# Kernel tuning notes

Measured on AMD Instinct MI355X. Metric: run time of the kernel, lower is better.

Reference implementation:

```python
import jax, jax.numpy as jnp
import numpy as np

B, N, IN_DIM, HID = 16, 2048, 128, 128
EPS = 1e-5


def _layer(x, W, b, g, beta):
    # x: (B, N, d_in) -> (B, N, HID)
    h = jnp.einsum('bnd,dh->bnh', x, W) + b
    mu = jnp.mean(h, axis=-1, keepdims=True)
    var = jnp.mean((h - mu) ** 2, axis=-1, keepdims=True)
    h = (h - mu) * jax.lax.rsqrt(var + EPS) * g + beta
    return jax.nn.relu(h)


def setup_inputs() -> dict:
    key = jax.random.key(0)
    ks = jax.random.split(key, 8)
    x = jax.random.normal(ks[0], (B, N, IN_DIM), dtype=jnp.float32)
    adj = jax.random.uniform(ks[1], (B, N, N), dtype=jnp.float32)
    inp = {'x': x, 'adj': adj}
    dims = [IN_DIM, HID, HID]
    for i in range(3):
        d_in = dims[i]
        scale = 1.0 / np.sqrt(d_in)
        inp[f'W{i}'] = jax.random.uniform(ks[2 + i], (d_in, HID), dtype=jnp.float32, minval=-scale, maxval=scale)
        inp[f'b{i}'] = jax.random.uniform(ks[5 + i], (HID,), dtype=jnp.float32, minval=-scale, maxval=scale)
        inp[f'g{i}'] = jnp.ones((HID,), dtype=jnp.float32)
        inp[f'be{i}'] = jnp.zeros((HID,), dtype=jnp.float32)
    return inp


def reference(x, adj, W0, b0, g0, be0, W1, b1, g1, be1, W2, b2, g2, be2):
    params = [(W0, b0, g0, be0), (W1, b1, g1, be1), (W2, b2, g2, be2)]
    h = x
    for (W, b, g, beta) in params:
        h_agg = jnp.einsum('bnm,bmd->bnd', adj, h)  # dense adjacency aggregation
        h = _layer(h_agg, W, b, g, beta)
    return h
```

## Files before the change

kernel.cpp:

```cpp
#include <hip/hip_runtime.h>
#include <hip/hip_bf16.h>

typedef __bf16 bf16;
typedef __bf16 bf16x4 __attribute__((ext_vector_type(4)));
typedef __bf16 bf16x8 __attribute__((ext_vector_type(8)));
typedef float  f32x2  __attribute__((ext_vector_type(2)));
typedef float  f32x4  __attribute__((ext_vector_type(4)));

static constexpr int NB  = 16;
static constexpr int NN  = 2048;
static constexpr int HID = 128;

__device__ __forceinline__ void gload_lds16(const bf16* g, bf16* l) {
    __builtin_amdgcn_global_load_lds(
        (const __attribute__((address_space(1))) unsigned int*)g,
        (__attribute__((address_space(3))) unsigned int*)l, 16, 0, 0);
}

__global__ __launch_bounds__(256) void prep_wt(const float* __restrict__ W0,
                                               const float* __restrict__ W1,
                                               const float* __restrict__ W2,
                                               bf16* __restrict__ WT) {
    int l = blockIdx.x;
    const float* W = (l == 0) ? W0 : (l == 1) ? W1 : W2;
    bf16* out = WT + l * 128 * 128;
    int tid = threadIdx.x;
#pragma unroll
    for (int i = 0; i < 64; ++i) {
        int idx = i * 256 + tid;
        int k = idx >> 7, n = idx & 127;
        out[n * 128 + k] = (bf16)W[idx];
    }
}

__global__ __launch_bounds__(256) void prep_xt(const float* __restrict__ x,
                                               bf16* __restrict__ xT) {
    __shared__ bf16 T[128 * 136];
    const int blk = blockIdx.x;
    const int b = blk >> 4, node0 = (blk & 15) * 128;
    const int tid = threadIdx.x;
    const float* xb = x + ((size_t)b * NN + node0) * HID;
#pragma unroll
    for (int i = 0; i < 64; ++i) {
        int idx = i * 256 + tid;
        int node = idx >> 7, hid = idx & 127;
        T[hid * 136 + node] = (bf16)xb[(size_t)node * HID + hid];
    }
    __syncthreads();
    bf16* ob = xT + (size_t)b * HID * NN + node0;
#pragma unroll
    for (int i = 0; i < 8; ++i) {
        int flat = i * 2048 + tid * 8;
        int hid = flat >> 7, node = flat & 127;
        *(bf16x8*)(ob + (size_t)hid * NN + node) = *(const bf16x8*)(T + hid * 136 + node);
    }
}

template<int AMODE>
__global__ __launch_bounds__(256, 2) void big_gemm(const float* __restrict__ Af,
                                                   bf16* __restrict__ adjB,
                                                   const bf16* __restrict__ Bt,
                                                   bf16* __restrict__ g) {
    __shared__ bf16 As[64 * 64];
    __shared__ bf16 Bs[128 * 64];

    const int tid  = threadIdx.x;
    const int wave = tid >> 6, lane = tid & 63;
    const int c0 = lane & 15, q = lane >> 4;
    const int m0 = blockIdx.x * 64;
    const int b  = blockIdx.z;
    const size_t abase = (size_t)b * NN * NN;
    const bf16* Btb = Bt + (size_t)b * HID * NN;
    const int wm = wave >> 1, wn = wave & 1;

    f32x4 acc[2][4] = {};

    int prow[4], pcb[4];
#pragma unroll
    for (int j = 0; j < 4; ++j) {
        int p = j * 256 + wave * 64 + lane;
        prow[j] = p >> 3;
        pcb[j]  = (p & 7) ^ (prow[j] & 7);
    }
    const int ldsbase = wave * 512;

    for (int kk = 0; kk < 32; ++kk) {
        const int k0 = kk * 64;
        if constexpr (AMODE == 1) {
#pragma unroll
            for (int j = 0; j < 2; ++j) {
                int gi = j * 256 + tid;
                int grow = gi >> 3, gcb = gi & 7;
                const float* src = Af + abase + (size_t)(m0 + grow) * NN + k0 + gcb * 8;
                f32x4 a  = *(const f32x4*)src;
                f32x4 b2 = *(const f32x4*)(src + 4);
                bf16x8 o = {(bf16)a.x, (bf16)a.y, (bf16)a.z, (bf16)a.w,
                            (bf16)b2.x, (bf16)b2.y, (bf16)b2.z, (bf16)b2.w};
                *(bf16x8*)(As + (grow * 8 + (gcb ^ (grow & 7))) * 8) = o;
                *(bf16x8*)(adjB + abase + (size_t)(m0 + grow) * NN + k0 + gcb * 8) = o;
            }
        } else {
#pragma unroll
            for (int j = 0; j < 2; ++j)
                gload_lds16(adjB + abase + (size_t)(m0 + prow[j]) * NN + k0 + pcb[j] * 8,
                            As + j * 2048 + ldsbase);
        }
#pragma unroll
        for (int j = 0; j < 4; ++j)
            gload_lds16(Btb + (size_t)prow[j] * NN + k0 + pcb[j] * 8,
                        Bs + j * 2048 + ldsbase);
        __syncthreads();
#pragma unroll
        for (int ks = 0; ks < 2; ++ks) {
            bf16x8 af[2], bfr[4];
#pragma unroll
            for (int mt = 0; mt < 2; ++mt) {
                int row = wm * 32 + mt * 16 + c0;
                int cb  = (ks * 4 + q) ^ (row & 7);
                af[mt] = *(const bf16x8*)(As + row * 64 + cb * 8);
            }
#pragma unroll
            for (int nt = 0; nt < 4; ++nt) {
                int row = wn * 64 + nt * 16 + c0;
                int cb  = (ks * 4 + q) ^ (row & 7);
                bfr[nt] = *(const bf16x8*)(Bs + row * 64 + cb * 8);
            }
#pragma unroll
            for (int mt = 0; mt < 2; ++mt)
#pragma unroll
                for (int nt = 0; nt < 4; ++nt)
                    acc[mt][nt] = __builtin_amdgcn_mfma_f32_16x16x32_bf16(af[mt], bfr[nt], acc[mt][nt], 0, 0, 0);
        }
        __syncthreads();
    }

    bf16* gb = g + ((size_t)b * NN + m0) * HID;
#pragma unroll
    for (int mt = 0; mt < 2; ++mt)
#pragma unroll
        for (int r = 0; r < 4; ++r) {
            int m = wm * 32 + mt * 16 + q * 4 + r;
#pragma unroll
            for (int nt = 0; nt < 4; ++nt) {
                int n = wn * 64 + nt * 16 + c0;
                gb[(size_t)m * HID + n] = (bf16)acc[mt][nt][r];
            }
        }
}

template<bool FINAL>
__global__ __launch_bounds__(256) void small_ln(const bf16* __restrict__ gin,
                                                const bf16* __restrict__ WT,
                                                const float* __restrict__ bias,
                                                const float* __restrict__ gamma,
                                                const float* __restrict__ betap,
                                                bf16* __restrict__ hT,
                                                float* __restrict__ outF) {
    __shared__ bf16 smem[2 * 128 * 72];
    bf16* As = smem;
    bf16* Bs = smem + 128 * 72;

    const int tid  = threadIdx.x;
    const int wave = tid >> 6, lane = tid & 63;
    const int c0 = lane & 15, q = lane >> 4;
    const int blk = blockIdx.x;
    const int row_g0 = blk * 128;

    f32x4 acc[2][8] = {};

    for (int kk = 0; kk < 2; ++kk) {
        const int k0 = kk * 64;
#pragma unroll
        for (int i = 0; i < 4; ++i) {
            int flat = i * 2048 + tid * 8;
            int row = flat >> 6, col = flat & 63;
            bf16x8 v = *(const bf16x8*)(gin + (size_t)(row_g0 + row) * HID + k0 + col);
            *(bf16x8*)(As + row * 72 + col) = v;
        }
#pragma unroll
        for (int i = 0; i < 4; ++i) {
            int flat = i * 2048 + tid * 8;
            int row = flat >> 6, col = flat & 63;
            bf16x8 v = *(const bf16x8*)(WT + (size_t)row * 128 + k0 + col);
            *(bf16x8*)(Bs + row * 72 + col) = v;
        }
        __syncthreads();
#pragma unroll
        for (int ks = 0; ks < 2; ++ks) {
            bf16x8 af[2];
#pragma unroll
            for (int mt = 0; mt < 2; ++mt)
                af[mt] = *(const bf16x8*)(As + (wave * 32 + mt * 16 + c0) * 72 + ks * 32 + q * 8);
#pragma unroll
            for (int nt = 0; nt < 8; ++nt) {
                bf16x8 bfr = *(const bf16x8*)(Bs + (nt * 16 + c0) * 72 + ks * 32 + q * 8);
#pragma unroll
                for (int mt = 0; mt < 2; ++mt)
                    acc[mt][nt] = __builtin_amdgcn_mfma_f32_16x16x32_bf16(af[mt], bfr, acc[mt][nt], 0, 0, 0);
            }
        }
        __syncthreads();
    }

    float bv[8], gv[8], bev[8];
#pragma unroll
    for (int nt = 0; nt < 8; ++nt) {
        int n = nt * 16 + c0;
        bv[nt] = bias[n]; gv[nt] = gamma[n]; bev[nt] = betap[n];
    }
    bf16* Cs = smem;
#pragma unroll
    for (int mt = 0; mt < 2; ++mt) {
#pragma unroll
        for (int r = 0; r < 4; ++r) {
            float v[8], s1 = 0.f, s2 = 0.f;
#pragma unroll
            for (int nt = 0; nt < 8; ++nt) {
                float xv = acc[mt][nt][r] + bv[nt];
                v[nt] = xv; s1 += xv; s2 += xv * xv;
            }
#pragma unroll
            for (int off = 1; off < 16; off <<= 1) {
                s1 += __shfl_xor(s1, off);
                s2 += __shfl_xor(s2, off);
            }
            float mu  = s1 * (1.f / 128.f);
            float var = s2 * (1.f / 128.f) - mu * mu;
            float rs  = rsqrtf(var + 1e-5f);
            int m = wave * 32 + mt * 16 + q * 4 + r;
            if constexpr (FINAL) {
                size_t rowoff = ((size_t)row_g0 + m) * HID;
#pragma unroll
                for (int nt = 0; nt < 8; ++nt) {
                    float o = fmaxf((v[nt] - mu) * rs * gv[nt] + bev[nt], 0.f);
                    outF[rowoff + nt * 16 + c0] = o;
                }
            } else {
#pragma unroll
                for (int nt = 0; nt < 8; ++nt) {
                    float o = fmaxf((v[nt] - mu) * rs * gv[nt] + bev[nt], 0.f);
                    Cs[(nt * 16 + c0) * 136 + m] = (bf16)o;
                }
            }
        }
    }
    if constexpr (!FINAL) {
        __syncthreads();
        const int b = blk >> 4, row0 = (blk & 15) * 128;
        bf16* outp = hT + (size_t)b * HID * NN;
#pragma unroll
        for (int i = 0; i < 8; ++i) {
            int flat = i * 2048 + tid * 8;
            int n = flat >> 7, mm = flat & 127;
            *(bf16x8*)(outp + (size_t)n * NN + row0 + mm) = *(const bf16x8*)(Cs + n * 136 + mm);
        }
    }
}

extern "C" void kernel_launch(void* const* d_in, const int* in_sizes, int n_in,
                              void* d_out, int out_size, void* d_ws, size_t ws_size,
                              hipStream_t stream) {
    const float* x   = (const float*)d_in[0];
    const float* adj = (const float*)d_in[1];
    const float* W[3]  = {(const float*)d_in[2],  (const float*)d_in[6],  (const float*)d_in[10]};
    const float* bb[3] = {(const float*)d_in[3],  (const float*)d_in[7],  (const float*)d_in[11]};
    const float* gg[3] = {(const float*)d_in[4],  (const float*)d_in[8],  (const float*)d_in[12]};
    const float* be[3] = {(const float*)d_in[5],  (const float*)d_in[9],  (const float*)d_in[13]};

    char* ws = (char*)d_ws;
    size_t off = 0;
    auto alloc = [&](size_t bytes) { char* p = ws + off; off = (off + bytes + 255) & ~(size_t)255; return p; };
    bf16* WT   = (bf16*)alloc((size_t)3 * 128 * 128 * 2);
    bf16* xT   = (bf16*)alloc((size_t)NB * HID * NN * 2);
    bf16* hT   = (bf16*)alloc((size_t)NB * HID * NN * 2);
    bf16* gbuf = (bf16*)alloc((size_t)NB * NN * HID * 2);
    bf16* adjB = (bf16*)alloc((size_t)NB * NN * NN * 2);

    float* outF = (float*)d_out;

    prep_wt<<<3, 256, 0, stream>>>(W[0], W[1], W[2], WT);
    prep_xt<<<256, 256, 0, stream>>>(x, xT);

    dim3 bg(32, 1, 16);
    big_gemm<1><<<bg, 256, 0, stream>>>(adj, adjB, xT, gbuf);
    small_ln<false><<<256, 256, 0, stream>>>(gbuf, WT, bb[0], gg[0], be[0], hT, nullptr);
    big_gemm<2><<<bg, 256, 0, stream>>>(adj, adjB, hT, gbuf);
    small_ln<false><<<256, 256, 0, stream>>>(gbuf, WT + 128 * 128, bb[1], gg[1], be[1], hT, nullptr);
    big_gemm<2><<<bg, 256, 0, stream>>>(adj, adjB, hT, gbuf);
    small_ln<true><<<256, 256, 0, stream>>>(gbuf, WT + 2 * 128 * 128, bb[2], gg[2], be[2], nullptr, outF);
}
```

Baseline: 552.4 us.

## Double-buffer big_gemm LDS tiles and remap blocks so each XCD owns two batches

The adjacency GEMM now keeps two LDS stages, so the next K tile's global loads (async for bf16 adj and B, register-staged for the fp32 first pass) are issued before computing on the current tile. This is meant to hide load latency that was previously serialized behind a barrier. The grid also becomes 1D with a mapping that puts blocks of the same two batches on one XCD, aiming for better L2 reuse of the B operand. Doubling LDS use to 48KB per block may cut how many blocks fit per CU, and the fp32 path holds more registers across the compute step.

Result: no change. 555.5 us (+0.6%).

```diff
diff --git a/kernel.cpp b/kernel.cpp
--- a/kernel.cpp
+++ b/kernel.cpp
@@ -61,14 +61,18 @@
                                                    bf16* __restrict__ adjB,
                                                    const bf16* __restrict__ Bt,
                                                    bf16* __restrict__ g) {
-    __shared__ bf16 As[64 * 64];
-    __shared__ bf16 Bs[128 * 64];
+    __shared__ bf16 As[2][64 * 64];
+    __shared__ bf16 Bs[2][128 * 64];
 
     const int tid  = threadIdx.x;
     const int wave = tid >> 6, lane = tid & 63;
     const int c0 = lane & 15, q = lane >> 4;
-    const int m0 = blockIdx.x * 64;
-    const int b  = blockIdx.z;
+
+    const int blk = blockIdx.x;
+    const int xcd = blk & 7, jj = blk >> 3;
+    const int b   = xcd * 2 + (jj & 1);
+    const int m0  = (jj >> 1) * 64;
+
     const size_t abase = (size_t)b * NN * NN;
     const bf16* Btb = Bt + (size_t)b * HID * NN;
     const int wm = wave >> 1, wn = wave & 1;
@@ -84,32 +88,44 @@
     }
     const int ldsbase = wave * 512;
 
-    for (int kk = 0; kk < 32; ++kk) {
-        const int k0 = kk * 64;
-        if constexpr (AMODE == 1) {
-#pragma unroll
-            for (int j = 0; j < 2; ++j) {
-                int gi = j * 256 + tid;
-                int grow = gi >> 3, gcb = gi & 7;
-                const float* src = Af + abase + (size_t)(m0 + grow) * NN + k0 + gcb * 8;
-                f32x4 a  = *(const f32x4*)src;
-                f32x4 b2 = *(const f32x4*)(src + 4);
-                bf16x8 o = {(bf16)a.x, (bf16)a.y, (bf16)a.z, (bf16)a.w,
-                            (bf16)b2.x, (bf16)b2.y, (bf16)b2.z, (bf16)b2.w};
-                *(bf16x8*)(As + (grow * 8 + (gcb ^ (grow & 7))) * 8) = o;
-                *(bf16x8*)(adjB + abase + (size_t)(m0 + grow) * NN + k0 + gcb * 8) = o;
-            }
-        } else {
-#pragma unroll
-            for (int j = 0; j < 2; ++j)
-                gload_lds16(adjB + abase + (size_t)(m0 + prow[j]) * NN + k0 + pcb[j] * 8,
-                            As + j * 2048 + ldsbase);
-        }
+    int grow_[2], gcb_[2];
+#pragma unroll
+    for (int j = 0; j < 2; ++j) {
+        int gi = j * 256 + tid;
+        grow_[j] = gi >> 3;
+        gcb_[j]  = gi & 7;
+    }
+
+    auto stageB = [&](int buf, int k0) {
 #pragma unroll
         for (int j = 0; j < 4; ++j)
             gload_lds16(Btb + (size_t)prow[j] * NN + k0 + pcb[j] * 8,
-                        Bs + j * 2048 + ldsbase);
-        __syncthreads();
+                        &Bs[buf][j * 2048 + ldsbase]);
+    };
+    auto stageA_async = [&](int buf, int k0) {
+#pragma unroll
+        for (int j = 0; j < 2; ++j)
+            gload_lds16(adjB + abase + (size_t)(m0 + prow[j]) * NN + k0 + pcb[j] * 8,
+                        &As[buf][j * 2048 + ldsbase]);
+    };
+    auto loadA_f32 = [&](int k0, f32x4* va, f32x4* vb) {
+#pragma unroll
+        for (int j = 0; j < 2; ++j) {
+            const float* src = Af + abase + (size_t)(m0 + grow_[j]) * NN + k0 + gcb_[j] * 8;
+            va[j] = *(const f32x4*)src;
+            vb[j] = *(const f32x4*)(src + 4);
+        }
+    };
+    auto writeA = [&](int buf, int k0, const f32x4* va, const f32x4* vb) {
+#pragma unroll
+        for (int j = 0; j < 2; ++j) {
+            bf16x8 o = {(bf16)va[j].x, (bf16)va[j].y, (bf16)va[j].z, (bf16)va[j].w,
+                        (bf16)vb[j].x, (bf16)vb[j].y, (bf16)vb[j].z, (bf16)vb[j].w};
+            *(bf16x8*)(&As[buf][(grow_[j] * 8 + (gcb_[j] ^ (grow_[j] & 7))) * 8]) = o;
+            *(bf16x8*)(adjB + abase + (size_t)(m0 + grow_[j]) * NN + k0 + gcb_[j] * 8) = o;
+        }
+    };
+    auto compute = [&](int buf) {
 #pragma unroll
         for (int ks = 0; ks < 2; ++ks) {
             bf16x8 af[2], bfr[4];
@@ -117,13 +133,13 @@
             for (int mt = 0; mt < 2; ++mt) {
                 int row = wm * 32 + mt * 16 + c0;
                 int cb  = (ks * 4 + q) ^ (row & 7);
-                af[mt] = *(const bf16x8*)(As + row * 64 + cb * 8);
+                af[mt] = *(const bf16x8*)(&As[buf][row * 64 + cb * 8]);
             }
 #pragma unroll
             for (int nt = 0; nt < 4; ++nt) {
                 int row = wn * 64 + nt * 16 + c0;
                 int cb  = (ks * 4 + q) ^ (row & 7);
-                bfr[nt] = *(const bf16x8*)(Bs + row * 64 + cb * 8);
+                bfr[nt] = *(const bf16x8*)(&Bs[buf][row * 64 + cb * 8]);
             }
 #pragma unroll
             for (int mt = 0; mt < 2; ++mt)
@@ -131,7 +147,39 @@
                 for (int nt = 0; nt < 4; ++nt)
                     acc[mt][nt] = __builtin_amdgcn_mfma_f32_16x16x32_bf16(af[mt], bfr[nt], acc[mt][nt], 0, 0, 0);
         }
+    };
+
+    f32x4 va[2], vb[2];
+    if constexpr (AMODE == 1) {
+        loadA_f32(0, va, vb);
+        stageB(0, 0);
+        writeA(0, 0, va, vb);
+    } else {
+        stageA_async(0, 0);
+        stageB(0, 0);
+    }
+    __syncthreads();
+
+    int cur = 0;
+    for (int kk = 0; kk < 32; ++kk) {
+        const int k1 = (kk + 1) * 64;
+        if constexpr (AMODE == 1) {
+            if (kk < 31) {
+                loadA_f32(k1, va, vb);
+                stageB(cur ^ 1, k1);
+            }
+            compute(cur);
+            if (kk < 31)
+                writeA(cur ^ 1, k1, va, vb);
+        } else {
+            if (kk < 31) {
+                stageA_async(cur ^ 1, k1);
+                stageB(cur ^ 1, k1);
+            }
+            compute(cur);
+        }
         __syncthreads();
+        cur ^= 1;
     }
 
     bf16* gb = g + ((size_t)b * NN + m0) * HID;
@@ -281,11 +329,10 @@
     prep_wt<<<3, 256, 0, stream>>>(W[0], W[1], W[2], WT);
     prep_xt<<<256, 256, 0, stream>>>(x, xT);
 
-    dim3 bg(32, 1, 16);
-    big_gemm<1><<<bg, 256, 0, stream>>>(adj, adjB, xT, gbuf);
+    big_gemm<1><<<512, 256, 0, stream>>>(adj, adjB, xT, gbuf);
     small_ln<false><<<256, 256, 0, stream>>>(gbuf, WT, bb[0], gg[0], be[0], hT, nullptr);
-    big_gemm<2><<<bg, 256, 0, stream>>>(adj, adjB, hT, gbuf);
+    big_gemm<2><<<512, 256, 0, stream>>>(adj, adjB, hT, gbuf);
     small_ln<false><<<256, 256, 0, stream>>>(gbuf, WT + 128 * 128, bb[1], gg[1], be[1], hT, nullptr);
-    big_gemm<2><<<bg, 256, 0, stream>>>(adj, adjB, hT, gbuf);
+    big_gemm<2><<<512, 256, 0, stream>>>(adj, adjB, hT, gbuf);
     small_ln<true><<<256, 256, 0, stream>>>(gbuf, WT + 2 * 128 * 128, bb[2], gg[2], be[2], nullptr, outF);
 }
```

## Fuse aggregation GEMM with weight GEMM and LayerNorm per layer, pre-swizzled tiles

Applied to the files above, without the earlier changes.

Merges the adjacency aggregation GEMM and the small weight-GEMM plus LayerNorm/ReLU into one kernel per layer, so the intermediate g tensor stays in LDS instead of going through global memory. Operands are stored in a pre-tiled, pre-swizzled layout so each 64-wide K chunk is one contiguous block that global_load_lds can copy directly. Loads are double-buffered with explicit vmcnt waits, and blocks are mapped by XCD for cache locality. Tiles grow to 128 rows with 512 threads, which raises LDS use and may lower occupancy.

Result: faster. 494.7 us (-10.4%).

```diff
diff --git a/kernel.cpp b/kernel.cpp
--- a/kernel.cpp
+++ b/kernel.cpp
@@ -2,9 +2,7 @@
 #include <hip/hip_bf16.h>
 
 typedef __bf16 bf16;
-typedef __bf16 bf16x4 __attribute__((ext_vector_type(4)));
 typedef __bf16 bf16x8 __attribute__((ext_vector_type(8)));
-typedef float  f32x2  __attribute__((ext_vector_type(2)));
 typedef float  f32x4  __attribute__((ext_vector_type(4)));
 
 static constexpr int NB  = 16;
@@ -16,25 +14,32 @@
         (const __attribute__((address_space(1))) unsigned int*)g,
         (__attribute__((address_space(3))) unsigned int*)l, 16, 0, 0);
 }
+__device__ __forceinline__ void memfence() { asm volatile("" ::: "memory"); }
+
 
 __global__ __launch_bounds__(256) void prep_wt(const float* __restrict__ W0,
                                                const float* __restrict__ W1,
                                                const float* __restrict__ W2,
-                                               bf16* __restrict__ WT) {
+                                               bf16* __restrict__ WTg) {
     int l = blockIdx.x;
     const float* W = (l == 0) ? W0 : (l == 1) ? W1 : W2;
-    bf16* out = WT + l * 128 * 128;
+    bf16* out = WTg + l * 16384;
     int tid = threadIdx.x;
 #pragma unroll
-    for (int i = 0; i < 64; ++i) {
-        int idx = i * 256 + tid;
-        int k = idx >> 7, n = idx & 127;
-        out[n * 128 + k] = (bf16)W[idx];
+    for (int i = 0; i < 8; ++i) {
+        int p = i * 256 + tid;
+        int n = p >> 4, half = (p >> 3) & 1, cs = p & 7;
+        int kc = cs ^ (n & 7);
+        int kbase = half * 64 + kc * 8;
+        bf16x8 o;
+#pragma unroll
+        for (int r = 0; r < 8; ++r) o[r] = (bf16)W[(kbase + r) * 128 + n];
+        *(bf16x8*)(out + p * 8) = o;
     }
 }
 
 __global__ __launch_bounds__(256) void prep_xt(const float* __restrict__ x,
-                                               bf16* __restrict__ xT) {
+                                               bf16* __restrict__ xTt) {
     __shared__ bf16 T[128 * 136];
     const int blk = blockIdx.x;
     const int b = blk >> 4, node0 = (blk & 15) * 128;
@@ -47,212 +52,220 @@
         T[hid * 136 + node] = (bf16)xb[(size_t)node * HID + hid];
     }
     __syncthreads();
-    bf16* ob = xT + (size_t)b * HID * NN + node0;
 #pragma unroll
     for (int i = 0; i < 8; ++i) {
-        int flat = i * 2048 + tid * 8;
-        int hid = flat >> 7, node = flat & 127;
-        *(bf16x8*)(ob + (size_t)hid * NN + node) = *(const bf16x8*)(T + hid * 136 + node);
-    }
-}
-
-template<int AMODE>
-__global__ __launch_bounds__(256, 2) void big_gemm(const float* __restrict__ Af,
-                                                   bf16* __restrict__ adjB,
-                                                   const bf16* __restrict__ Bt,
-                                                   bf16* __restrict__ g) {
-    __shared__ bf16 As[64 * 64];
-    __shared__ bf16 Bs[128 * 64];
-
-    const int tid  = threadIdx.x;
-    const int wave = tid >> 6, lane = tid & 63;
+        int p = i * 256 + tid;
+        int half = p >> 10, p1 = p & 1023;
+        int n = p1 >> 3, cs = p1 & 7, c = cs ^ (n & 7), m = half * 64 + c * 8;
+        *(bf16x8*)(xTt + ((size_t)b * 32 + (node0 >> 6) + half) * 8192 + p1 * 8)
+            = *(const bf16x8*)(T + n * 136 + m);
+    }
+}
+
+template<int AMODE, bool FINAL>
+__global__ __launch_bounds__(512, 2) void fused_layer(
+        const float* __restrict__ Af, bf16* __restrict__ adjT,
+        const bf16* __restrict__ Bt, const bf16* __restrict__ WTg,
+        const float* __restrict__ bias, const float* __restrict__ gam,
+        const float* __restrict__ bet, bf16* __restrict__ hOut,
+        float* __restrict__ outF) {
+    __shared__ __align__(16) bf16 lds[49152];
+    bf16* WTl = lds + 32768;
+
+    const int tid = threadIdx.x, wave = tid >> 6, lane = tid & 63;
     const int c0 = lane & 15, q = lane >> 4;
-    const int m0 = blockIdx.x * 64;
-    const int b  = blockIdx.z;
-    const size_t abase = (size_t)b * NN * NN;
-    const bf16* Btb = Bt + (size_t)b * HID * NN;
+    const int blk = blockIdx.x, xcd = blk & 7, jj = blk >> 3;
+    const int b = xcd * 2 + (jj & 1);
+    const int mtile = jj >> 1, m0 = mtile * 128;
     const int wm = wave >> 1, wn = wave & 1;
 
+    const bf16* Btb = Bt + (size_t)b * 32 * 8192;
+    bf16* Atl = adjT + ((size_t)b * 16 + mtile) * 32 * 8192;
+
     f32x4 acc[2][4] = {};
 
-    int prow[4], pcb[4];
 #pragma unroll
     for (int j = 0; j < 4; ++j) {
-        int p = j * 256 + wave * 64 + lane;
-        prow[j] = p >> 3;
-        pcb[j]  = (p & 7) ^ (prow[j] & 7);
-    }
-    const int ldsbase = wave * 512;
-
-    for (int kk = 0; kk < 32; ++kk) {
-        const int k0 = kk * 64;
-        if constexpr (AMODE == 1) {
-#pragma unroll
-            for (int j = 0; j < 2; ++j) {
-                int gi = j * 256 + tid;
-                int grow = gi >> 3, gcb = gi & 7;
-                const float* src = Af + abase + (size_t)(m0 + grow) * NN + k0 + gcb * 8;
-                f32x4 a  = *(const f32x4*)src;
-                f32x4 b2 = *(const f32x4*)(src + 4);
-                bf16x8 o = {(bf16)a.x, (bf16)a.y, (bf16)a.z, (bf16)a.w,
-                            (bf16)b2.x, (bf16)b2.y, (bf16)b2.z, (bf16)b2.w};
-                *(bf16x8*)(As + (grow * 8 + (gcb ^ (grow & 7))) * 8) = o;
-                *(bf16x8*)(adjB + abase + (size_t)(m0 + grow) * NN + k0 + gcb * 8) = o;
-            }
-        } else {
-#pragma unroll
-            for (int j = 0; j < 2; ++j)
-                gload_lds16(adjB + abase + (size_t)(m0 + prow[j]) * NN + k0 + pcb[j] * 8,
-                            As + j * 2048 + ldsbase);
-        }
-#pragma unroll
-        for (int j = 0; j < 4; ++j)
-            gload_lds16(Btb + (size_t)prow[j] * NN + k0 + pcb[j] * 8,
-                        Bs + j * 2048 + ldsbase);
-        __syncthreads();
+        int cb = j * 512 + wave * 64;
+        gload_lds16(WTg + (size_t)(cb + lane) * 8, WTl + cb * 8);
+    }
+
+    auto stageA2 = [&](int buf, int kk) {
+#pragma unroll
+        for (int j = 0; j < 2; ++j) {
+            int cb = j * 512 + wave * 64;
+            gload_lds16(Atl + (size_t)kk * 8192 + (size_t)(cb + lane) * 8,
+                        lds + buf * 16384 + cb * 8);
+        }
+    };
+    auto stageB2 = [&](int buf, int kk) {
+#pragma unroll
+        for (int j = 0; j < 2; ++j) {
+            int cb = j * 512 + wave * 64;
+            gload_lds16(Btb + (size_t)kk * 8192 + (size_t)(cb + lane) * 8,
+                        lds + buf * 16384 + 8192 + cb * 8);
+        }
+    };
+    auto compute = [&](int buf) {
+        const bf16* As = lds + buf * 16384;
+        const bf16* Bs = As + 8192;
 #pragma unroll
         for (int ks = 0; ks < 2; ++ks) {
-            bf16x8 af[2], bfr[4];
+            bf16x8 af[2], bf_[4];
 #pragma unroll
             for (int mt = 0; mt < 2; ++mt) {
                 int row = wm * 32 + mt * 16 + c0;
-                int cb  = (ks * 4 + q) ^ (row & 7);
+                int cb = (ks * 4 + q) ^ (row & 7);
                 af[mt] = *(const bf16x8*)(As + row * 64 + cb * 8);
             }
 #pragma unroll
             for (int nt = 0; nt < 4; ++nt) {
                 int row = wn * 64 + nt * 16 + c0;
-                int cb  = (ks * 4 + q) ^ (row & 7);
-                bfr[nt] = *(const bf16x8*)(Bs + row * 64 + cb * 8);
+                int cb = (ks * 4 + q) ^ (row & 7);
+                bf_[nt] = *(const bf16x8*)(Bs + row * 64 + cb * 8);
             }
 #pragma unroll
             for (int mt = 0; mt < 2; ++mt)
 #pragma unroll
                 for (int nt = 0; nt < 4; ++nt)
-                    acc[mt][nt] = __builtin_amdgcn_mfma_f32_16x16x32_bf16(af[mt], bfr[nt], acc[mt][nt], 0, 0, 0);
-        }
+                    acc[mt][nt] = __builtin_amdgcn_mfma_f32_16x16x32_bf16(
+                        af[mt], bf_[nt], acc[mt][nt], 0, 0, 0);
+        }
+    };
+
+    if constexpr (AMODE == 1) {
+        int grow[2], gcb[2];
+#pragma unroll
+        for (int j = 0; j < 2; ++j) {
+            int gi = j * 512 + tid;
+            grow[j] = gi >> 3; gcb[j] = gi & 7;
+        }
+        f32x4 va[2], vb[2];
+        auto loadA = [&](int kk) {
+#pragma unroll
+            for (int j = 0; j < 2; ++j) {
+                const float* s = Af + (size_t)b * NN * NN
+                               + (size_t)(m0 + grow[j]) * NN + kk * 64 + gcb[j] * 8;
+                va[j] = *(const f32x4*)s;
+                vb[j] = *(const f32x4*)(s + 4);
+            }
+        };
+        auto writeA = [&](int buf, int kk) {
+#pragma unroll
+            for (int j = 0; j < 2; ++j) {
+                bf16x8 o = {(bf16)va[j].x, (bf16)va[j].y, (bf16)va[j].z, (bf16)va[j].w,
+                            (bf16)vb[j].x, (bf16)vb[j].y, (bf16)vb[j].z, (bf16)vb[j].w};
+                int ch = grow[j] * 8 + (gcb[j] ^ (grow[j] & 7));
+                *(bf16x8*)(lds + buf * 16384 + ch * 8) = o;
+                *(bf16x8*)(Atl + (size_t)kk * 8192 + ch * 8) = o;
+            }
+        };
+        loadA(0); stageB2(0, 0); writeA(0, 0);
         __syncthreads();
-    }
-
-    bf16* gb = g + ((size_t)b * NN + m0) * HID;
+        int cur = 0;
+        for (int kk = 0; kk < 32; ++kk) {
+            if (kk < 31) { loadA(kk + 1); stageB2(cur ^ 1, kk + 1); }
+            compute(cur);
+            if (kk < 31) writeA(cur ^ 1, kk + 1);
+            __syncthreads();
+            cur ^= 1;
+        }
+    } else {
+        stageA2(0, 0); stageB2(0, 0);
+        stageA2(1, 1); stageB2(1, 1);
+#pragma unroll 1
+        for (int kk = 0; kk < 32; ++kk) {
+            if (kk < 31) asm volatile("s_waitcnt vmcnt(4)" ::: "memory");
+            else         asm volatile("s_waitcnt vmcnt(0)" ::: "memory");
+            __builtin_amdgcn_s_barrier();
+            memfence();
+            compute(kk & 1);
+            memfence();
+            __builtin_amdgcn_s_barrier();
+            if (kk < 30) { stageA2(kk & 1, kk + 2); stageB2(kk & 1, kk + 2); }
+        }
+        __syncthreads();
+    }
+
+    bf16* G = lds;
 #pragma unroll
     for (int mt = 0; mt < 2; ++mt)
 #pragma unroll
         for (int r = 0; r < 4; ++r) {
-            int m = wm * 32 + mt * 16 + q * 4 + r;
+            int row = wm * 32 + mt * 16 + q * 4 + r;
 #pragma unroll
             for (int nt = 0; nt < 4; ++nt) {
-                int n = wn * 64 + nt * 16 + c0;
-                gb[(size_t)m * HID + n] = (bf16)acc[mt][nt][r];
-            }
-        }
-}
-
-template<bool FINAL>
-__global__ __launch_bounds__(256) void small_ln(const bf16* __restrict__ gin,
-                                                const bf16* __restrict__ WT,
-                                                const float* __restrict__ bias,
-                                                const float* __restrict__ gamma,
-                                                const float* __restrict__ betap,
-                                                bf16* __restrict__ hT,
-                                                float* __restrict__ outF) {
-    __shared__ bf16 smem[2 * 128 * 72];
-    bf16* As = smem;
-    bf16* Bs = smem + 128 * 72;
-
-    const int tid  = threadIdx.x;
-    const int wave = tid >> 6, lane = tid & 63;
-    const int c0 = lane & 15, q = lane >> 4;
-    const int blk = blockIdx.x;
-    const int row_g0 = blk * 128;
-
-    f32x4 acc[2][8] = {};
-
-    for (int kk = 0; kk < 2; ++kk) {
-        const int k0 = kk * 64;
-#pragma unroll
-        for (int i = 0; i < 4; ++i) {
-            int flat = i * 2048 + tid * 8;
-            int row = flat >> 6, col = flat & 63;
-            bf16x8 v = *(const bf16x8*)(gin + (size_t)(row_g0 + row) * HID + k0 + col);
-            *(bf16x8*)(As + row * 72 + col) = v;
-        }
-#pragma unroll
-        for (int i = 0; i < 4; ++i) {
-            int flat = i * 2048 + tid * 8;
-            int row = flat >> 6, col = flat & 63;
-            bf16x8 v = *(const bf16x8*)(WT + (size_t)row * 128 + k0 + col);
-            *(bf16x8*)(Bs + row * 72 + col) = v;
-        }
-        __syncthreads();
-#pragma unroll
-        for (int ks = 0; ks < 2; ++ks) {
-            bf16x8 af[2];
-#pragma unroll
-            for (int mt = 0; mt < 2; ++mt)
-                af[mt] = *(const bf16x8*)(As + (wave * 32 + mt * 16 + c0) * 72 + ks * 32 + q * 8);
+                int col = wn * 64 + nt * 16 + c0;
+                G[row * 136 + col] = (bf16)acc[mt][nt][r];
+            }
+        }
+    __syncthreads();
+
+    f32x4 a2[8] = {};
+    {
+        const int gr = wave * 16 + c0;
+#pragma unroll
+        for (int ks = 0; ks < 4; ++ks) {
+            bf16x8 af = *(const bf16x8*)(G + gr * 136 + ks * 32 + q * 8);
 #pragma unroll
             for (int nt = 0; nt < 8; ++nt) {
-                bf16x8 bfr = *(const bf16x8*)(Bs + (nt * 16 + c0) * 72 + ks * 32 + q * 8);
-#pragma unroll
-                for (int mt = 0; mt < 2; ++mt)
-                    acc[mt][nt] = __builtin_amdgcn_mfma_f32_16x16x32_bf16(af[mt], bfr, acc[mt][nt], 0, 0, 0);
-            }
-        }
-        __syncthreads();
-    }
-
-    float bv[8], gv[8], bev[8];
+                int n = nt * 16 + c0;
+                int ch = n * 16 + (ks >> 1) * 8 + ((((ks & 1) << 2) | q) ^ (n & 7));
+                bf16x8 bw = *(const bf16x8*)(WTl + ch * 8);
+                a2[nt] = __builtin_amdgcn_mfma_f32_16x16x32_bf16(af, bw, a2[nt], 0, 0, 0);
+            }
+        }
+    }
+
+    float bv[8], gv[8], ev[8];
 #pragma unroll
     for (int nt = 0; nt < 8; ++nt) {
         int n = nt * 16 + c0;
-        bv[nt] = bias[n]; gv[nt] = gamma[n]; bev[nt] = betap[n];
-    }
-    bf16* Cs = smem;
-#pragma unroll
-    for (int mt = 0; mt < 2; ++mt) {
-#pragma unroll
-        for (int r = 0; r < 4; ++r) {
-            float v[8], s1 = 0.f, s2 = 0.f;
+        bv[nt] = bias[n]; gv[nt] = gam[n]; ev[nt] = bet[n];
+    }
+    bf16* Cs = lds;
+    if constexpr (!FINAL) __syncthreads();
+#pragma unroll
+    for (int r = 0; r < 4; ++r) {
+        float v[8], s1 = 0.f, s2 = 0.f;
+#pragma unroll
+        for (int nt = 0; nt < 8; ++nt) {
+            float xv = a2[nt][r] + bv[nt];
+            v[nt] = xv; s1 += xv; s2 += xv * xv;
+        }
+#pragma unroll
+        for (int off = 1; off < 16; off <<= 1) {
+            s1 += __shfl_xor(s1, off);
+            s2 += __shfl_xor(s2, off);
+        }
+        float mu = s1 * (1.f / 128.f);
+        float var = s2 * (1.f / 128.f) - mu * mu;
+        float rs = rsqrtf(var + 1e-5f);
+        int row = wave * 16 + q * 4 + r;
+        if constexpr (FINAL) {
+            size_t ro = ((size_t)b * NN + m0 + row) * HID;
 #pragma unroll
             for (int nt = 0; nt < 8; ++nt) {
-                float xv = acc[mt][nt][r] + bv[nt];
-                v[nt] = xv; s1 += xv; s2 += xv * xv;
-            }
-#pragma unroll
-            for (int off = 1; off < 16; off <<= 1) {
-                s1 += __shfl_xor(s1, off);
-                s2 += __shfl_xor(s2, off);
-            }
-            float mu  = s1 * (1.f / 128.f);
-            float var = s2 * (1.f / 128.f) - mu * mu;
-            float rs  = rsqrtf(var + 1e-5f);
-            int m = wave * 32 + mt * 16 + q * 4 + r;
-            if constexpr (FINAL) {
-                size_t rowoff = ((size_t)row_g0 + m) * HID;
-#pragma unroll
-                for (int nt = 0; nt < 8; ++nt) {
-                    float o = fmaxf((v[nt] - mu) * rs * gv[nt] + bev[nt], 0.f);
-                    outF[rowoff + nt * 16 + c0] = o;
-                }
-            } else {
-#pragma unroll
-                for (int nt = 0; nt < 8; ++nt) {
-                    float o = fmaxf((v[nt] - mu) * rs * gv[nt] + bev[nt], 0.f);
-                    Cs[(nt * 16 + c0) * 136 + m] = (bf16)o;
-                }
+                float o = fmaxf((v[nt] - mu) * rs * gv[nt] + ev[nt], 0.f);
+                outF[ro + nt * 16 + c0] = o;
+            }
+        } else {
+#pragma unroll
+            for (int nt = 0; nt < 8; ++nt) {
+                float o = fmaxf((v[nt] - mu) * rs * gv[nt] + ev[nt], 0.f);
+                Cs[(nt * 16 + c0) * 136 + row] = (bf16)o;
             }
         }
     }
     if constexpr (!FINAL) {
         __syncthreads();
-        const int b = blk >> 4, row0 = (blk & 15) * 128;
-        bf16* outp = hT + (size_t)b * HID * NN;
-#pragma unroll
-        for (int i = 0; i < 8; ++i) {
-            int flat = i * 2048 + tid * 8;
-            int n = flat >> 7, mm = flat & 127;
-            *(bf16x8*)(outp + (size_t)n * NN + row0 + mm) = *(const bf16x8*)(Cs + n * 136 + mm);
+#pragma unroll
+        for (int i = 0; i < 4; ++i) {
+            int p = i * 512 + tid;
+            int half = p >> 10, p1 = p & 1023;
+            int n = p1 >> 3, cs = p1 & 7, c = cs ^ (n & 7), m = half * 64 + c * 8;
+            *(bf16x8*)(hOut + ((size_t)b * 32 + mtile * 2 + half) * 8192 + p1 * 8)
+                = *(const bf16x8*)(Cs + n * 136 + m);
         }
     }
 }
@@ -269,23 +282,24 @@
 
     char* ws = (char*)d_ws;
     size_t off = 0;
-    auto alloc = [&](size_t bytes) { char* p = ws + off; off = (off + bytes + 255) & ~(size_t)255; return p; };
-    bf16* WT   = (bf16*)alloc((size_t)3 * 128 * 128 * 2);
-    bf16* xT   = (bf16*)alloc((size_t)NB * HID * NN * 2);
-    bf16* hT   = (bf16*)alloc((size_t)NB * HID * NN * 2);
-    bf16* gbuf = (bf16*)alloc((size_t)NB * NN * HID * 2);
-    bf16* adjB = (bf16*)alloc((size_t)NB * NN * NN * 2);
+    auto alloc = [&](size_t bytes) {
+        char* p = ws + off; off = (off + bytes + 255) & ~(size_t)255; return p;
+    };
+    bf16* WTg  = (bf16*)alloc((size_t)3 * 16384 * 2);
+    bf16* xTt  = (bf16*)alloc((size_t)NB * 32 * 8192 * 2);
+    bf16* hT0  = (bf16*)alloc((size_t)NB * 32 * 8192 * 2);
+    bf16* hT1  = (bf16*)alloc((size_t)NB * 32 * 8192 * 2);
+    bf16* adjT = (bf16*)alloc((size_t)NB * 16 * 32 * 8192 * 2);
 
     float* outF = (float*)d_out;
 
-    prep_wt<<<3, 256, 0, stream>>>(W[0], W[1], W[2], WT);
-    prep_xt<<<256, 256, 0, stream>>>(x, xT);
-
-    dim3 bg(32, 1, 16);
-    big_gemm<1><<<bg, 256, 0, stream>>>(adj, adjB, xT, gbuf);
-    small_ln<false><<<256, 256, 0, stream>>>(gbuf, WT, bb[0], gg[0], be[0], hT, nullptr);
-    big_gemm<2><<<bg, 256, 0, stream>>>(adj, adjB, hT, gbuf);
-    small_ln<false><<<256, 256, 0, stream>>>(gbuf, WT + 128 * 128, bb[1], gg[1], be[1], hT, nullptr);
-    big_gemm<2><<<bg, 256, 0, stream>>>(adj, adjB, hT, gbuf);
-    small_ln<true><<<256, 256, 0, stream>>>(gbuf, WT + 2 * 128 * 128, bb[2], gg[2], be[2], nullptr, outF);
-}
+    prep_wt<<<3, 256, 0, stream>>>(W[0], W[1], W[2], WTg);
+    prep_xt<<<256, 256, 0, stream>>>(x, xTt);
+
+    fused_layer<1, false><<<256, 512, 0, stream>>>(adj, adjT, xTt, WTg,
+                                                   bb[0], gg[0], be[0], hT0, nullptr);
+    fused_layer<2, false><<<256, 512, 0, stream>>>(adj, adjT, hT0, WTg + 16384,
+                                                   bb[1], gg[1], be[1], hT1, nullptr);
+    fused_layer<2, true ><<<256, 512, 0, stream>>>(adj, adjT, hT1, WTg + 2 * 16384,
+                                                   bb[2], gg[2], be[2], nullptr, outF);
+}
```
